# Kernel tuning notes

Hardware: AMD Instinct MI355X
Metric: run time of the kernel (lower is better)

The kernel has to match this reference:

```python
import jax, jax.numpy as jnp
import numpy as np

B, S, D = 2, 2048, 2048
H, KV, HD = 32, 8, 64
REP = H // KV
THETA = 10000.0


def _rope_tables(seq_len, head_dim, dtype):
    inv_freq = 1.0 / (THETA ** (jnp.arange(0, head_dim, 2, dtype=jnp.float32) / head_dim))
    t = jnp.arange(seq_len, dtype=jnp.float32)
    freqs = jnp.outer(t, inv_freq)  # [S, HD/2]
    return jnp.cos(freqs).astype(dtype), jnp.sin(freqs).astype(dtype)


def _apply_rope(x, cos, sin):
    # x: [B, S, nh, HD]; cos/sin: [S, HD/2] -> broadcast [1, S, 1, HD/2]
    c = cos[None, :, None, :]
    s = sin[None, :, None, :]
    x1, x2 = x[..., : HD // 2], x[..., HD // 2:]
    return jnp.concatenate([x1 * c - x2 * s, x1 * s + x2 * c], axis=-1)


def setup_inputs() -> dict:
    key = jax.random.key(0)
    ks = jax.random.split(key, 5)
    x = jax.random.normal(ks[0], (B, S, D), dtype=jnp.float32)
    wq = jax.random.normal(ks[1], (D, H * HD), dtype=jnp.float32) * 0.02
    wk = jax.random.normal(ks[2], (D, KV * HD), dtype=jnp.float32) * 0.02
    wv = jax.random.normal(ks[3], (D, KV * HD), dtype=jnp.float32) * 0.02
    wo = jax.random.normal(ks[4], (H * HD, D), dtype=jnp.float32) * 0.02
    return {"x": x, "wq": wq, "wk": wk, "wv": wv, "wo": wo}


def reference(x, wq, wk, wv, wo):
    b, s, _ = x.shape
    q = (x @ wq).reshape(b, s, H, HD)
    k = (x @ wk).reshape(b, s, KV, HD)
    v = (x @ wv).reshape(b, s, KV, HD)

    cos, sin = _rope_tables(s, HD, x.dtype)
    q = _apply_rope(q, cos, sin)
    k = _apply_rope(k, cos, sin)

    # GQA: group query heads by KV head instead of repeating K/V (same math).
    qg = q.reshape(b, s, KV, REP, HD)  # [B,S,G,R,HD]
    scale = HD ** -0.5
    # scores: [B, G, R, Sq, Sk]
    scores = jnp.einsum("bsgrd,btgd->bgrst", qg, k) * scale
    causal = jnp.tril(jnp.ones((s, s), dtype=bool))
    scores = jnp.where(causal[None, None, None], scores, jnp.finfo(scores.dtype).min)
    probs = jax.nn.softmax(scores, axis=-1)
    out = jnp.einsum("bgrst,btgd->bsgrd", probs, v)  # [B,S,G,R,HD]
    out = out.reshape(b, s, H * HD)
    return out @ wo
```

## Files before the change

kernel.cpp:

```cpp
#include <hip/hip_runtime.h>

#define S_LEN 2048
#define NH 32
#define NKV 8
#define HEADD 64
#define DMODEL 2048
#define NQKV 3072

typedef float f32x4 __attribute__((ext_vector_type(4)));
typedef float f32x16 __attribute__((ext_vector_type(16)));
typedef short s16x8 __attribute__((ext_vector_type(8)));
typedef int   i32x4 __attribute__((ext_vector_type(4)));
typedef unsigned short u16;
typedef u16 u16x4 __attribute__((ext_vector_type(4)));

__device__ __forceinline__ float b2f(u16 u) {
  unsigned int x = ((unsigned int)u) << 16;
  float f;
  __builtin_memcpy(&f, &x, 4);
  return f;
}
__device__ __forceinline__ u16 f2b(float f) {
  unsigned int x;
  __builtin_memcpy(&x, &f, 4);
  unsigned int r = x + 0x7fffu + ((x >> 16) & 1u);
  return (u16)(r >> 16);
}
__device__ __forceinline__ unsigned fbits(float f) {
  unsigned x; __builtin_memcpy(&x, &f, 4); return x;
}

__device__ __forceinline__ void gload_lds16(const u16* g, u16* l) {
  __builtin_amdgcn_global_load_lds((const __attribute__((address_space(1))) void*)g,
                                   (__attribute__((address_space(3))) void*)l, 16, 0, 0);
}

__global__ void cast_x_kernel(const float* __restrict__ src, u16* __restrict__ dst) {
  int i = (blockIdx.x * 256 + threadIdx.x) * 4;
  f32x4 v = *(const f32x4*)(src + i);
  u16x4 o;
  o[0] = f2b(v[0]); o[1] = f2b(v[1]); o[2] = f2b(v[2]); o[3] = f2b(v[3]);
  *(u16x4*)(dst + i) = o;
}

__global__ void transpose_cast(const float* __restrict__ src, u16* __restrict__ dst, int N, int K) {
  __shared__ float tile[32][33];
  int n0 = blockIdx.x * 32, k0 = blockIdx.y * 32;
  int tx = threadIdx.x, ty = threadIdx.y;
#pragma unroll
  for (int i = 0; i < 32; i += 8)
    tile[ty + i][tx] = src[(size_t)(k0 + ty + i) * N + n0 + tx];
  __syncthreads();
#pragma unroll
  for (int i = 0; i < 32; i += 8)
    dst[(size_t)(n0 + ty + i) * K + k0 + tx] = f2b(tile[tx][ty + i]);
}

__global__ __launch_bounds__(256) void gemm_bt(
    const u16* __restrict__ A, const u16* __restrict__ Bt, void* __restrict__ Cout,
    int M, int N, int K, int writeF32) {
  __shared__ __align__(16) u16 As[128 * 32];
  __shared__ __align__(16) u16 Bs[128 * 32];

  int nb = N >> 7;
  int m0 = (blockIdx.x / nb) << 7;
  int n0 = (blockIdx.x % nb) << 7;
  int tid = threadIdx.x;
  int lane = tid & 63;
  int w4 = tid >> 6;
  int l15 = lane & 15;
  int quad = lane >> 4;
  int wm = (w4 >> 1) << 6;
  int wn = (w4 & 1) << 6;

  const u16* gA0 = A  + (size_t)(m0 + w4 * 32 + (lane >> 2)) * K + ((lane & 3) << 3);
  const u16* gA1 = gA0 + (size_t)16 * K;
  const u16* gB0 = Bt + (size_t)(n0 + w4 * 32 + (lane >> 2)) * K + ((lane & 3) << 3);
  const u16* gB1 = gB0 + (size_t)16 * K;
  u16* lA0 = &As[w4 * 1024];
  u16* lA1 = &As[w4 * 1024 + 512];
  u16* lB0 = &Bs[w4 * 1024];
  u16* lB1 = &Bs[w4 * 1024 + 512];

  f32x4 acc[4][4] = {};

  for (int k0 = 0; k0 < K; k0 += 32) {
    __syncthreads();
    gload_lds16(gA0 + k0, lA0);
    gload_lds16(gA1 + k0, lA1);
    gload_lds16(gB0 + k0, lB0);
    gload_lds16(gB1 + k0, lB1);
    __syncthreads();

    s16x8 af[4], bf[4];
#pragma unroll
    for (int i = 0; i < 4; i++)
      af[i] = *(const s16x8*)&As[(wm + i * 16 + l15) * 32 + (quad << 3)];
#pragma unroll
    for (int i = 0; i < 4; i++)
      bf[i] = *(const s16x8*)&Bs[(wn + i * 16 + l15) * 32 + (quad << 3)];
#pragma unroll
    for (int mi = 0; mi < 4; mi++)
#pragma unroll
      for (int ni = 0; ni < 4; ni++)
        acc[mi][ni] = __builtin_amdgcn_mfma_f32_16x16x32_bf16(af[mi], bf[ni], acc[mi][ni], 0, 0, 0);
  }

#pragma unroll
  for (int mi = 0; mi < 4; mi++)
#pragma unroll
    for (int ni = 0; ni < 4; ni++)
#pragma unroll
      for (int r = 0; r < 4; r++) {
        int row = m0 + wm + mi * 16 + (quad << 2) + r;
        int col = n0 + wn + ni * 16 + l15;
        float v = acc[mi][ni][r];
        if (writeF32) ((float*)Cout)[(size_t)row * N + col] = v;
        else ((u16*)Cout)[(size_t)row * N + col] = f2b(v);
      }
}

__global__ void rope_kernel(u16* __restrict__ qkv) {
  int row = blockIdx.x;
  int s = row & (S_LEN - 1);
  u16* p = qkv + (size_t)row * NQKV;
  int t = threadIdx.x;
  int d = t & 31;
  int hh = t >> 5;
  float inv_freq = exp2f(-(float)d * (13.287712379549449f / 32.0f));
  float ang = (float)s * inv_freq;
  float sn, cs;
  sincosf(ang, &sn, &cs);
  const float QSCALE = 0.18033688011112042f;
#pragma unroll
  for (int i = 0; i < 4; i++) {
    int base = (hh + (i << 3)) * HEADD + d;
    float x1 = b2f(p[base]);
    float x2 = b2f(p[base + 32]);
    p[base]      = f2b((x1 * cs - x2 * sn) * QSCALE);
    p[base + 32] = f2b((x1 * sn + x2 * cs) * QSCALE);
  }
  {
    int base = DMODEL + hh * HEADD + d;
    float x1 = b2f(p[base]);
    float x2 = b2f(p[base + 32]);
    p[base]      = f2b(x1 * cs - x2 * sn);
    p[base + 32] = f2b(x1 * sn + x2 * cs);
  }
}

__global__ void vtrans_kernel(const u16* __restrict__ qkv, u16* __restrict__ Vt) {
  __shared__ __align__(16) u16 tile[64][72];
  int bid = blockIdx.x;
  int st = bid & 31;
  int g  = (bid >> 5) & 7;
  int b  = bid >> 8;
  int tid = threadIdx.x;
  int r = tid >> 2;
  int c = (tid & 3) << 4;
  const u16* src = qkv + (size_t)(b * S_LEN + st * 64 + r) * NQKV + 2560 + g * 64 + c;
  *(i32x4*)&tile[r][c]     = *(const i32x4*)src;
  *(i32x4*)&tile[r][c + 8] = *(const i32x4*)(src + 8);
  __syncthreads();
  u16* dst = Vt + (size_t)((b * 8 + g) * 64 + r) * S_LEN + st * 64 + c;
  u16 tmp[16];
#pragma unroll
  for (int j = 0; j < 16; j++) tmp[j] = tile[c + j][r];
  *(i32x4*)dst       = *(i32x4*)&tmp[0];
  *(i32x4*)(dst + 8) = *(i32x4*)&tmp[8];
}

__global__ __launch_bounds__(64) void kvpack_kernel(const u16* __restrict__ qkv,
                                                    const u16* __restrict__ Vt,
                                                    u16* __restrict__ Kp,
                                                    u16* __restrict__ Vp) {
  int bid = blockIdx.x;
  int kb = bid & 63;
  int bg = bid >> 6;
  int g = bg & 7;
  int b = bg >> 3;
  int lane = threadIdx.x;
  int l31 = lane & 31;
  int h2 = lane >> 5;

  const u16* kq = qkv + (size_t)(b * S_LEN + kb * 32 + l31) * NQKV + DMODEL + g * 64 + h2 * 8;
  u16* kdst = Kp + ((size_t)bid * 4) * 512 + lane * 8;
#pragma unroll
  for (int t = 0; t < 4; t++)
    *(i32x4*)(kdst + t * 512) = *(const i32x4*)(kq + t * 16);

  const u16* vq = Vt + (size_t)(bg * 64 + l31) * S_LEN + kb * 32 + h2 * 8;
  u16* vdst = Vp + ((size_t)bid * 4) * 512 + lane * 8;
  *(i32x4*)(vdst)        = *(const i32x4*)vq;
  *(i32x4*)(vdst + 512)  = *(const i32x4*)(vq + 16);
  *(i32x4*)(vdst + 1024) = *(const i32x4*)(vq + (size_t)32 * S_LEN);
  *(i32x4*)(vdst + 1536) = *(const i32x4*)(vq + (size_t)32 * S_LEN + 16);
}

__global__ __launch_bounds__(64) void attn_kernel(const u16* __restrict__ qkv,
                                                  const u16* __restrict__ Kp,
                                                  const u16* __restrict__ Vp,
                                                  u16* __restrict__ out) {
  int bid = blockIdx.x;
  int bh = bid & 63;
  int qb = 63 - (bid >> 6);
  int h = bh & 31;
  int b = bh >> 5;
  int g = h >> 2;
  int bg = b * 8 + g;
  int lane = threadIdx.x;
  int l31 = lane & 31;
  int h2 = lane >> 5;
  int q0 = qb << 5;

  const u16* qp = qkv + (size_t)(b * S_LEN + q0 + l31) * NQKV + h * HEADD + h2 * 8;
  s16x8 qf[4];
#pragma unroll
  for (int t = 0; t < 4; t++) qf[t] = *(const s16x8*)(qp + t * 16);

  const u16* kp = Kp + ((size_t)bg * 64) * 2048 + lane * 8;
  const u16* vp = Vp + ((size_t)bg * 64) * 2048 + lane * 8;

  float m_i = -1e30f, l_i = 0.f;
  f32x16 acc[2] = {};

  s16x8 kfa[4], vfa[4], kfb[4], vfb[4];

  auto loadkv = [&](int kb, s16x8 (&kf)[4], s16x8 (&vf)[4]) {
    const u16* kpp = kp + (size_t)kb * 2048;
    const u16* vpp = vp + (size_t)kb * 2048;
#pragma unroll
    for (int t = 0; t < 4; t++) {
      kf[t] = *(const s16x8*)(kpp + t * 512);
      vf[t] = *(const s16x8*)(vpp + t * 512);
    }
  };

  auto compute = [&](int kb, s16x8 (&kf)[4], s16x8 (&vf)[4]) {
    f32x16 sc = {};
    __builtin_amdgcn_s_setprio(1);
#pragma unroll
    for (int t = 0; t < 4; t++)
      sc = __builtin_amdgcn_mfma_f32_32x32x16_bf16(kf[t], qf[t], sc, 0, 0, 0);
    __builtin_amdgcn_s_setprio(0);

    float sv[16];
#pragma unroll
    for (int j = 0; j < 16; j++) sv[j] = sc[j];

    if (kb == qb) {
      int qg = q0 + l31;
#pragma unroll
      for (int j = 0; j < 16; j++) {
        int kg = kb * 32 + (j & 3) + ((j >> 2) << 3) + (h2 << 2);
        if (kg > qg) sv[j] = -1e30f;
      }
    }

    float a0 = fmaxf(fmaxf(sv[0], sv[1]), sv[2]);
    float a1 = fmaxf(fmaxf(sv[3], sv[4]), sv[5]);
    float a2 = fmaxf(fmaxf(sv[6], sv[7]), sv[8]);
    float a3 = fmaxf(fmaxf(sv[9], sv[10]), sv[11]);
    float a4 = fmaxf(fmaxf(sv[12], sv[13]), sv[14]);
    float b0m = fmaxf(fmaxf(a0, a1), a2);
    float b1m = fmaxf(fmaxf(a3, a4), sv[15]);
    float mx = fmaxf(b0m, b1m);
    mx = fmaxf(mx, __shfl_xor(mx, 32));

    if (__any(mx > m_i + 4.0f)) {
      float m_new = fmaxf(m_i, mx);
      float alpha = __builtin_amdgcn_exp2f(m_i - m_new);
      m_i = m_new;
      l_i *= alpha;
#pragma unroll
      for (int dt = 0; dt < 2; dt++)
#pragma unroll
        for (int j = 0; j < 16; j++) acc[dt][j] *= alpha;
    }

    float e[16];
#pragma unroll
    for (int j = 0; j < 16; j++) e[j] = __builtin_amdgcn_exp2f(sv[j] - m_i);

    float ps = (((e[0] + e[1]) + (e[2] + e[3])) + ((e[4] + e[5]) + (e[6] + e[7])))
             + (((e[8] + e[9]) + (e[10] + e[11])) + ((e[12] + e[13]) + (e[14] + e[15])));
    ps += __shfl_xor(ps, 32);
    l_i += ps;

    unsigned Pk[8], Ex[8];
#pragma unroll
    for (int r = 0; r < 8; r++) {
      unsigned ae = fbits(e[2 * r]) + 0x8000u;
      unsigned ao = fbits(e[2 * r + 1]) + 0x8000u;
      Pk[r] = __builtin_amdgcn_perm(ao, ae, 0x07060302u);
    }
#pragma unroll
    for (int r = 0; r < 8; r++) Ex[r] = (unsigned)__shfl_xor((int)Pk[r], 32);

    unsigned B0u[4], B1u[4];
    B0u[0] = h2 ? Ex[2] : Pk[0];
    B0u[1] = h2 ? Ex[3] : Pk[1];
    B0u[2] = h2 ? Pk[2] : Ex[0];
    B0u[3] = h2 ? Pk[3] : Ex[1];
    B1u[0] = h2 ? Ex[6] : Pk[4];
    B1u[1] = h2 ? Ex[7] : Pk[5];
    B1u[2] = h2 ? Pk[6] : Ex[4];
    B1u[3] = h2 ? Pk[7] : Ex[5];
    s16x8 B0, B1;
    __builtin_memcpy(&B0, B0u, 16);
    __builtin_memcpy(&B1, B1u, 16);

    __builtin_amdgcn_s_setprio(1);
    acc[0] = __builtin_amdgcn_mfma_f32_32x32x16_bf16(vf[0], B0, acc[0], 0, 0, 0);
    acc[0] = __builtin_amdgcn_mfma_f32_32x32x16_bf16(vf[1], B1, acc[0], 0, 0, 0);
    acc[1] = __builtin_amdgcn_mfma_f32_32x32x16_bf16(vf[2], B0, acc[1], 0, 0, 0);
    acc[1] = __builtin_amdgcn_mfma_f32_32x32x16_bf16(vf[3], B1, acc[1], 0, 0, 0);
    __builtin_amdgcn_s_setprio(0);
  };

  loadkv(0, kfa, vfa);
  int kb = 0;
  while (true) {
    if (kb < qb) loadkv(kb + 1, kfb, vfb);
    compute(kb, kfa, vfa);
    if (++kb > qb) break;
    if (kb < qb) loadkv(kb + 1, kfa, vfa);
    compute(kb, kfb, vfb);
    if (++kb > qb) break;
  }

  float linv = 1.0f / l_i;
  u16* op = out + (size_t)(b * S_LEN + q0 + l31) * DMODEL + h * HEADD;
#pragma unroll
  for (int dt = 0; dt < 2; dt++)
#pragma unroll
    for (int rg = 0; rg < 4; rg++) {
      u16x4 t4;
#pragma unroll
      for (int j = 0; j < 4; j++) t4[j] = f2b(acc[dt][rg * 4 + j] * linv);
      *(u16x4*)(op + dt * 32 + rg * 8 + h2 * 4) = t4;
    }
}

extern "C" void kernel_launch(void* const* d_in, const int* in_sizes, int n_in,
                              void* d_out, int out_size, void* d_ws, size_t ws_size,
                              hipStream_t stream) {
  const float* x  = (const float*)d_in[0];
  const float* wq = (const float*)d_in[1];
  const float* wk = (const float*)d_in[2];
  const float* wv = (const float*)d_in[3];
  const float* wo = (const float*)d_in[4];

  char* ws = (char*)d_ws;
  u16* xb    = (u16*)ws;
  u16* wqkvT = (u16*)(ws + 16777216);
  u16* woT   = (u16*)(ws + 16777216 + 12582912);
  u16* qkv   = (u16*)(ws + 16777216 + 12582912 + 8388608);
  u16* attnb = xb;
  u16* Vt    = wqkvT;
  u16* Kp    = (u16*)(ws + 16777216 + 4194304);
  u16* Vp    = (u16*)(ws + 16777216 + 8388608);

  cast_x_kernel<<<8192, 256, 0, stream>>>(x, xb);
  dim3 tb(32, 8);
  transpose_cast<<<dim3(64, 64), tb, 0, stream>>>(wq, wqkvT, 2048, 2048);
  transpose_cast<<<dim3(16, 64), tb, 0, stream>>>(wk, wqkvT + (size_t)2048 * 2048, 512, 2048);
  transpose_cast<<<dim3(16, 64), tb, 0, stream>>>(wv, wqkvT + (size_t)2560 * 2048, 512, 2048);
  transpose_cast<<<dim3(64, 64), tb, 0, stream>>>(wo, woT, 2048, 2048);

  gemm_bt<<<768, 256, 0, stream>>>(xb, wqkvT, qkv, 4096, NQKV, 2048, 0);
  rope_kernel<<<4096, 256, 0, stream>>>(qkv);
  vtrans_kernel<<<512, 256, 0, stream>>>(qkv, Vt);
  kvpack_kernel<<<1024, 64, 0, stream>>>(qkv, Vt, Kp, Vp);
  attn_kernel<<<4096, 64, 0, stream>>>(qkv, Kp, Vp, attnb);
  gemm_bt<<<512, 256, 0, stream>>>(attnb, woT, d_out, 4096, 2048, 2048, 1);
}
```

Baseline: 333.7 us.

## Pipeline GEMM with 4-stage LDS ring, XOR swizzle, and XCD-aware block remap

Replaces the synchronous load-then-compute GEMM with a 4-buffer LDS ring that prefetches three K-steps ahead and uses explicit vmcnt waits, so global-to-LDS loads overlap MFMA work. It adds an XOR swizzle on the LDS layout to reduce bank conflicts on fragment reads. It also remaps block IDs across the 8 XCDs to improve L2 locality, and raises instruction priority around the MFMAs. K is now hardcoded to 2048 and the larger LDS footprint may reduce occupancy.

```diff
diff --git a/kernel.cpp b/kernel.cpp
--- a/kernel.cpp
+++ b/kernel.cpp
@@ -35,6 +35,10 @@
                                    (__attribute__((address_space(3))) void*)l, 16, 0, 0);
 }
 
+template<int N> __device__ __forceinline__ void wait_vm() {
+  asm volatile("s_waitcnt vmcnt(%0)" :: "n"(N) : "memory");
+}
+
 __global__ void cast_x_kernel(const float* __restrict__ src, u16* __restrict__ dst) {
   int i = (blockIdx.x * 256 + threadIdx.x) * 4;
   f32x4 v = *(const f32x4*)(src + i);
@@ -56,55 +60,96 @@
     dst[(size_t)(n0 + ty + i) * K + k0 + tx] = f2b(tile[tx][ty + i]);
 }
 
-__global__ __launch_bounds__(256) void gemm_bt(
+#define GQB_BODY(Q, STAGE, VMN)                                                   \
+  {                                                                               \
+    wait_vm<VMN>();                                                               \
+    __syncthreads();                                                              \
+    if (STAGE) {                                                                  \
+      gload_lds16(gA0, lA + ((Q + 3) & 3) * 8192);                                \
+      gload_lds16(gA1, lA + ((Q + 3) & 3) * 8192 + 2048);                         \
+      gload_lds16(gB0, lB + ((Q + 3) & 3) * 8192);                                \
+      gload_lds16(gB1, lB + ((Q + 3) & 3) * 8192 + 2048);                         \
+      gA0 += 32; gA1 += 32; gB0 += 32; gB1 += 32;                                 \
+    }                                                                             \
+    s16x8 af[4], bf[4];                                                           \
+    _Pragma("unroll")                                                             \
+    for (int i = 0; i < 4; i++) af[i] = *(const s16x8*)(sm + Q * 8192 + aoff[i]); \
+    _Pragma("unroll")                                                             \
+    for (int i = 0; i < 4; i++) bf[i] = *(const s16x8*)(sm + Q * 8192 + boff[i]); \
+    __builtin_amdgcn_s_setprio(1);                                                \
+    _Pragma("unroll")                                                             \
+    for (int mi = 0; mi < 4; mi++)                                                \
+      _Pragma("unroll")                                                           \
+      for (int ni = 0; ni < 4; ni++)                                              \
+        acc[mi][ni] = __builtin_amdgcn_mfma_f32_16x16x32_bf16(af[mi], bf[ni], acc[mi][ni], 0, 0, 0); \
+    __builtin_amdgcn_s_setprio(0);                                                \
+  }
+
+__global__ __launch_bounds__(256) void gemm_qb(
     const u16* __restrict__ A, const u16* __restrict__ Bt, void* __restrict__ Cout,
-    int M, int N, int K, int writeF32) {
-  __shared__ __align__(16) u16 As[128 * 32];
-  __shared__ __align__(16) u16 Bs[128 * 32];
+    int M, int N, int writeF32) {
+  __shared__ __align__(16) u16 sm[32768];
 
   int nb = N >> 7;
-  int m0 = (blockIdx.x / nb) << 7;
-  int n0 = (blockIdx.x % nb) << 7;
+  int nwg = (M >> 7) * nb;
+  int cpx = nwg >> 3;
+  int bid = ((int)blockIdx.x & 7) * cpx + ((int)blockIdx.x >> 3);
+  int m0 = (bid / nb) << 7;
+  int n0 = (bid % nb) << 7;
+
   int tid = threadIdx.x;
   int lane = tid & 63;
-  int w4 = tid >> 6;
+  int w = tid >> 6;
+  int wm = (w >> 1) << 6;
+  int wn = (w & 1) << 6;
   int l15 = lane & 15;
   int quad = lane >> 4;
-  int wm = (w4 >> 1) << 6;
-  int wn = (w4 & 1) << 6;
-
-  const u16* gA0 = A  + (size_t)(m0 + w4 * 32 + (lane >> 2)) * K + ((lane & 3) << 3);
-  const u16* gA1 = gA0 + (size_t)16 * K;
-  const u16* gB0 = Bt + (size_t)(n0 + w4 * 32 + (lane >> 2)) * K + ((lane & 3) << 3);
-  const u16* gB1 = gB0 + (size_t)16 * K;
-  u16* lA0 = &As[w4 * 1024];
-  u16* lA1 = &As[w4 * 1024 + 512];
-  u16* lB0 = &Bs[w4 * 1024];
-  u16* lB1 = &Bs[w4 * 1024 + 512];
+
+  int lr = lane >> 3;
+  int lc = lane & 7;
+  int slot = lc ^ lr;
+  int kc8 = (slot & 3) << 3;
+  int mrel0 = ((w * 8 + lr) << 1) + (slot >> 2);
+  int mrel1 = ((w * 8 + 32 + lr) << 1) + (slot >> 2);
+  const u16* gA0 = A  + (size_t)(m0 + mrel0) * 2048 + kc8;
+  const u16* gA1 = A  + (size_t)(m0 + mrel1) * 2048 + kc8;
+  const u16* gB0 = Bt + (size_t)(n0 + mrel0) * 2048 + kc8;
+  const u16* gB1 = Bt + (size_t)(n0 + mrel1) * 2048 + kc8;
+  u16* lA = sm + w * 512;
+  u16* lB = sm + 4096 + w * 512;
+
+  int rb = l15 >> 1;
+  int sl = (((((l15 & 1) << 2) | quad) ^ rb)) << 3;
+  int rbase = rb * 64 + sl;
+  int aoff[4], boff[4];
+#pragma unroll
+  for (int i = 0; i < 4; i++) {
+    aoff[i] = wm * 32 + i * 512 + rbase;
+    boff[i] = 4096 + wn * 32 + i * 512 + rbase;
+  }
 
   f32x4 acc[4][4] = {};
 
-  for (int k0 = 0; k0 < K; k0 += 32) {
-    __syncthreads();
-    gload_lds16(gA0 + k0, lA0);
-    gload_lds16(gA1 + k0, lA1);
-    gload_lds16(gB0 + k0, lB0);
-    gload_lds16(gB1 + k0, lB1);
-    __syncthreads();
-
-    s16x8 af[4], bf[4];
-#pragma unroll
-    for (int i = 0; i < 4; i++)
-      af[i] = *(const s16x8*)&As[(wm + i * 16 + l15) * 32 + (quad << 3)];
-#pragma unroll
-    for (int i = 0; i < 4; i++)
-      bf[i] = *(const s16x8*)&Bs[(wn + i * 16 + l15) * 32 + (quad << 3)];
-#pragma unroll
-    for (int mi = 0; mi < 4; mi++)
-#pragma unroll
-      for (int ni = 0; ni < 4; ni++)
-        acc[mi][ni] = __builtin_amdgcn_mfma_f32_16x16x32_bf16(af[mi], bf[ni], acc[mi][ni], 0, 0, 0);
-  }
+#pragma unroll
+  for (int pt = 0; pt < 3; pt++) {
+    gload_lds16(gA0, lA + pt * 8192);
+    gload_lds16(gA1, lA + pt * 8192 + 2048);
+    gload_lds16(gB0, lB + pt * 8192);
+    gload_lds16(gB1, lB + pt * 8192 + 2048);
+    gA0 += 32; gA1 += 32; gB0 += 32; gB1 += 32;
+  }
+
+#pragma unroll 1
+  for (int it = 0; it < 15; ++it) {
+    GQB_BODY(0, 1, 8)
+    GQB_BODY(1, 1, 8)
+    GQB_BODY(2, 1, 8)
+    GQB_BODY(3, 1, 8)
+  }
+  GQB_BODY(0, 1, 8)
+  GQB_BODY(1, 0, 8)
+  GQB_BODY(2, 0, 4)
+  GQB_BODY(3, 0, 0)
 
 #pragma unroll
   for (int mi = 0; mi < 4; mi++)
@@ -368,10 +413,10 @@
   transpose_cast<<<dim3(16, 64), tb, 0, stream>>>(wv, wqkvT + (size_t)2560 * 2048, 512, 2048);
   transpose_cast<<<dim3(64, 64), tb, 0, stream>>>(wo, woT, 2048, 2048);
 
-  gemm_bt<<<768, 256, 0, stream>>>(xb, wqkvT, qkv, 4096, NQKV, 2048, 0);
+  gemm_qb<<<768, 256, 0, stream>>>(xb, wqkvT, qkv, 4096, NQKV, 0);
   rope_kernel<<<4096, 256, 0, stream>>>(qkv);
   vtrans_kernel<<<512, 256, 0, stream>>>(qkv, Vt);
   kvpack_kernel<<<1024, 64, 0, stream>>>(qkv, Vt, Kp, Vp);
   attn_kernel<<<4096, 64, 0, stream>>>(qkv, Kp, Vp, attnb);
-  gemm_bt<<<512, 256, 0, stream>>>(attnb, woT, d_out, 4096, 2048, 2048, 1);
-}
+  gemm_qb<<<512, 256, 0, stream>>>(attnb, woT, d_out, 4096, 2048, 1);
+}
```

Result: faster. 321.0 us (-3.8%).
